# Kernel tuning notes

Measured on AMD Instinct MI355X. Metric: run time of the kernel, lower is better.

The kernel has to match this reference:

```python
import jax, jax.numpy as jnp
import numpy as np
from jax import lax

N = 100000   # n_nodes
E = 600000   # n_edges (no self loops by construction)
D = 128      # hidden_dim
L = 3        # n_hops
K = 5        # tail_k_threshold


def setup_inputs() -> dict:
    key = jax.random.key(0)
    ks = jax.random.split(key, 10)
    x = jax.random.normal(ks[0], (N, D), dtype=jnp.float32)
    src = jax.random.randint(ks[1], (E,), 0, N)
    off = jax.random.randint(ks[2], (E,), 1, N)
    dst = (src + off) % N  # guarantees dst != src (self loops removed in original)
    s = 1.0 / np.sqrt(D)
    def U(k, shape):
        return jax.random.uniform(k, shape, minval=-s, maxval=s, dtype=jnp.float32)
    return {
        "x": x,
        "G1": U(ks[3], (L, D, D)), "G2": U(ks[4], (L, D, D)),
        "B1": U(ks[5], (L, D, D)), "B2": U(ks[6], (L, D, D)),
        "R": U(ks[7], (L, D)),
        "edge_src": src, "edge_dst": dst,
    }


def _lrelu(v):
    return jax.nn.leaky_relu(v, 0.2)


def reference(x, G1, G2, B1, B2, R, edge_src, edge_dst):
    # row degrees of adj (A[src, dst] = 1)
    deg = jax.ops.segment_sum(jnp.ones(E, jnp.float32), edge_src, num_segments=N)
    inv_d = jnp.where(deg > 0, 1.0 / jnp.maximum(deg, 1.0), 0.0)   # left norm D^-1 A
    inv_d1 = 1.0 / (deg + 1.0)                                      # (A+I) left norm
    inv_d2 = 1.0 / (deg + 2.0)                                      # +1 virtual node
    w0, w1, w2 = inv_d[edge_src], inv_d1[edge_src], inv_d2[edge_src]
    head_mask = deg > K

    def spmm(w_edge, h):  # (D^-1 A) @ h via gather-scale-scatter
        return jax.ops.segment_sum(w_edge[:, None] * h[edge_dst], edge_src, num_segments=N)

    def propagate(head):
        h = x
        embs = [h]
        sups = []
        for l in range(L):
            nb = spmm(w0, h)
            ft = lax.stop_gradient(h)
            nbd = lax.stop_gradient(nb)
            gamma = _lrelu(ft @ G1[l].T + nbd @ G2[l].T) + 1.0
            beta = _lrelu(ft @ B1[l].T + nbd @ B2[l].T)
            m = ft + gamma * R[l] + beta - nbd   # missing_info (Relation, ablation=0)
            sups.append(m)
            if head:
                h = spmm(w1, h) + inv_d1[:, None] * h
            else:
                h = spmm(w2, h) + inv_d2[:, None] * h + m * inv_d2[:, None]
            embs.append(h)
        emb = jnp.mean(jnp.stack(embs, 0), 0)
        sup = jnp.mean(jnp.stack(sups, 0), 0)
        return emb, sup

    emb_h, _ = propagate(True)
    emb_t, _ = propagate(False)
    node_emb = jnp.where(head_mask[:, None], emb_h, emb_t)
    return node_emb
```

## Files before the change

### kernel.cpp

```cpp
#include <hip/hip_runtime.h>

#define N_NODES 100000
#define N_EDGES 600000
#define DIM 128
#define SCAN_B 1024
#define NCHUNK 98

typedef __attribute__((ext_vector_type(4))) float f32x4;
typedef __attribute__((ext_vector_type(8))) short bf16x8;
typedef __attribute__((ext_vector_type(4))) unsigned short u16x4;
typedef __attribute__((ext_vector_type(8))) unsigned short u16x8;

__device__ __forceinline__ unsigned short f2bf(float f) {
    union { float f; unsigned u; } cv; cv.f = f;
    unsigned r = (cv.u + 0x7FFFu + ((cv.u >> 16) & 1u)) >> 16;
    return (unsigned short)r;
}
__device__ __forceinline__ float bf2f(unsigned short v) {
    union { unsigned u; float f; } c; c.u = ((unsigned)v) << 16; return c.f;
}


__global__ void k_degree(const int* __restrict__ src, int* __restrict__ degi) {
    int e = blockIdx.x * 256 + threadIdx.x;
    if (e < N_EDGES) atomicAdd(&degi[src[e]], 1);
}

__global__ void k_chunksum(const int* __restrict__ degi, int* __restrict__ bsum) {
    __shared__ int sm[SCAN_B];
    int i = blockIdx.x * SCAN_B + threadIdx.x;
    sm[threadIdx.x] = (i < N_NODES) ? degi[i] : 0;
    __syncthreads();
    for (int s = SCAN_B / 2; s > 0; s >>= 1) {
        if (threadIdx.x < (unsigned)s) sm[threadIdx.x] += sm[threadIdx.x + s];
        __syncthreads();
    }
    if (threadIdx.x == 0) bsum[blockIdx.x] = sm[0];
}

__global__ void k_scanb(int* __restrict__ bsum, int nb) {
    __shared__ int sm[128];
    int t = threadIdx.x;
    int v = (t < nb) ? bsum[t] : 0;
    sm[t] = v; __syncthreads();
    for (int s = 1; s < 128; s <<= 1) {
        int a = (t >= s) ? sm[t - s] : 0;
        __syncthreads();
        sm[t] += a;
        __syncthreads();
    }
    if (t < nb) bsum[t] = sm[t] - v;
}

__global__ void k_rowptr(const int* __restrict__ degi, const int* __restrict__ bsum,
                         int* __restrict__ rowptr, int* __restrict__ cnt,
                         float* __restrict__ inv0, float* __restrict__ inv1,
                         float* __restrict__ inv2) {
    __shared__ int sm[SCAN_B];
    int i = blockIdx.x * SCAN_B + threadIdx.x;
    int v = (i < N_NODES) ? degi[i] : 0;
    sm[threadIdx.x] = v; __syncthreads();
    for (int s = 1; s < SCAN_B; s <<= 1) {
        int a = (threadIdx.x >= (unsigned)s) ? sm[threadIdx.x - s] : 0;
        __syncthreads();
        sm[threadIdx.x] += a;
        __syncthreads();
    }
    if (i < N_NODES) {
        int excl = bsum[blockIdx.x] + sm[threadIdx.x] - v;
        rowptr[i] = excl;
        cnt[i] = excl;
        float d = (float)v;
        inv0[i] = (v > 0) ? 1.0f / d : 0.0f;
        inv1[i] = 1.0f / (d + 1.0f);
        inv2[i] = 1.0f / (d + 2.0f);
    }
}

__global__ void k_fill(const int* __restrict__ src, const int* __restrict__ dst,
                       int* __restrict__ cnt, int* __restrict__ col) {
    int e = blockIdx.x * 256 + threadIdx.x;
    if (e < N_EDGES) {
        int pos = atomicAdd(&cnt[src[e]], 1);
        col[pos] = dst[e];
    }
}

__global__ void k_pack(const float* __restrict__ G1, const float* __restrict__ G2,
                       const float* __restrict__ B1, const float* __restrict__ B2,
                       short* __restrict__ Wp) {
    int idx = blockIdx.x * 256 + threadIdx.x;
    int j = idx & 7, lane = (idx >> 3) & 63, nt = (idx >> 9) & 15, kb = (idx >> 13) & 7, l = idx >> 16;
    int k = kb * 32 + (lane >> 4) * 8 + j;
    int n = nt * 16 + (lane & 15);
    float v;
    if (n < 128) {
        v = (k < 128) ? G1[(l * 128 + n) * 128 + k] : G2[(l * 128 + n) * 128 + (k - 128)];
    } else {
        int n2 = n - 128;
        v = (k < 128) ? B1[(l * 128 + n2) * 128 + k] : B2[(l * 128 + n2) * 128 + (k - 128)];
    }
    Wp[idx] = (short)f2bf(v);
}

__global__ void k_xcast(const float* __restrict__ x, unsigned short* __restrict__ xb) {
    int i = (blockIdx.x * 256 + threadIdx.x) * 4;
    f32x4 v = *(const f32x4*)(x + i);
    unsigned short o0 = f2bf(v[0]), o1 = f2bf(v[1]), o2 = f2bf(v[2]), o3 = f2bf(v[3]);
    unsigned long long pk = (unsigned long long)o0 | ((unsigned long long)o1 << 16)
                          | ((unsigned long long)o2 << 32) | ((unsigned long long)o3 << 48);
    *(unsigned long long*)(xb + i) = pk;
}


__device__ __forceinline__ void gather4(const u16x8* __restrict__ h8,
        const int* __restrict__ col, int start, int d, int lane, float* acc) {
    int c = lane & 15;
    int base = lane & 48;
    int dd = d < 16 ? d : 16;
    int idx = (c < dd) ? col[start + c] : 0;
    int dm = d;
    int tmx = __shfl_xor(dm, 16);
    dm = dm > tmx ? dm : tmx;
    tmx = __shfl_xor(dm, 32);
    dm = dm > tmx ? dm : tmx;
    int dmain = dm < 16 ? dm : 16;
    int e = 0;
    for (; e + 2 <= dmain; e += 2) {
        int c0 = __shfl(idx, base + e, 64);
        int c1 = __shfl(idx, base + e + 1, 64);
        if (e < d) {
            u16x8 v = h8[(size_t)c0 * 16 + c];
#pragma unroll
            for (int j = 0; j < 8; ++j) acc[j] += bf2f(v[j]);
        }
        if (e + 1 < d) {
            u16x8 v = h8[(size_t)c1 * 16 + c];
#pragma unroll
            for (int j = 0; j < 8; ++j) acc[j] += bf2f(v[j]);
        }
    }
    if (e < dmain) {
        int c0 = __shfl(idx, base + e, 64);
        if (e < d) {
            u16x8 v = h8[(size_t)c0 * 16 + c];
#pragma unroll
            for (int j = 0; j < 8; ++j) acc[j] += bf2f(v[j]);
        }
        ++e;
    }
    if (dm > 16) {
        for (; e < d; ++e) {
            int c0 = col[start + e];
            u16x8 v = h8[(size_t)c0 * 16 + c];
#pragma unroll
            for (int j = 0; j < 8; ++j) acc[j] += bf2f(v[j]);
        }
    }
}

__global__ __launch_bounds__(256) void k_agg0(
    const unsigned short* __restrict__ xb, unsigned short* __restrict__ Sb,
    unsigned short* __restrict__ hA, const float* __restrict__ inv1,
    const int* __restrict__ rowptr, const int* __restrict__ degi,
    const int* __restrict__ col)
{
    int lane = threadIdx.x & 63;
    int wid = (blockIdx.x * 256 + threadIdx.x) >> 6;
    int g = lane >> 4, c = lane & 15;
    int row = wid * 4 + g;
    int start = rowptr[row], d = degi[row];
    float acc[8] = {0,0,0,0,0,0,0,0};
    gather4((const u16x8*)xb, col, start, d, lane, acc);
    u16x8 hv = ((const u16x8*)xb)[(size_t)row * 16 + c];
    float w = inv1[row];
    u16x8 so, ho;
#pragma unroll
    for (int j = 0; j < 8; ++j) {
        so[j] = f2bf(acc[j]);
        ho[j] = f2bf(w * (acc[j] + bf2f(hv[j])));
    }
    ((u16x8*)Sb)[(size_t)row * 16 + c] = so;
    ((u16x8*)hA)[(size_t)row * 16 + c] = ho;
}

__global__ __launch_bounds__(256) void k_agg_head4(
    const unsigned short* __restrict__ hsrc, unsigned short* __restrict__ hnext,
    const unsigned short* __restrict__ xb, const unsigned short* __restrict__ h1b,
    float* __restrict__ outp, const float* __restrict__ inv1,
    const int* __restrict__ rowptr, const int* __restrict__ degi,
    const int* __restrict__ col, int final_hop)
{
    int lane = threadIdx.x & 63;
    int wid = (blockIdx.x * 256 + threadIdx.x) >> 6;
    int g = lane >> 4, c = lane & 15;
    int row = wid * 4 + g;
    int start = rowptr[row], d = degi[row];
    float acc[8] = {0,0,0,0,0,0,0,0};
    gather4((const u16x8*)hsrc, col, start, d, lane, acc);
    u16x8 hv = ((const u16x8*)hsrc)[(size_t)row * 16 + c];
    float w = inv1[row];
    float hn[8];
#pragma unroll
    for (int j = 0; j < 8; ++j) hn[j] = w * (acc[j] + bf2f(hv[j]));
    if (!final_hop) {
        u16x8 ho;
#pragma unroll
        for (int j = 0; j < 8; ++j) ho[j] = f2bf(hn[j]);
        ((u16x8*)hnext)[(size_t)row * 16 + c] = ho;
    } else {
        u16x8 xv = ((const u16x8*)xb)[(size_t)row * 16 + c];
        u16x8 h1 = ((const u16x8*)h1b)[(size_t)row * 16 + c];
        f32x4 e0, e1;
#pragma unroll
        for (int j = 0; j < 4; ++j)
            e0[j] = 0.25f * (bf2f(xv[j]) + bf2f(h1[j]) + bf2f(hv[j]) + hn[j]);
#pragma unroll
        for (int j = 0; j < 4; ++j)
            e1[j] = 0.25f * (bf2f(xv[4 + j]) + bf2f(h1[4 + j]) + bf2f(hv[4 + j]) + hn[4 + j]);
        float* op = outp + (size_t)row * DIM + c * 8;
        *(f32x4*)op = e0;
        *(f32x4*)(op + 4) = e1;
    }
}

__global__ __launch_bounds__(256) void k_agg_tail4(
    const unsigned short* __restrict__ hsrc, unsigned short* __restrict__ Sb,
    const int* __restrict__ rowptr, const int* __restrict__ degi,
    const int* __restrict__ col)
{
    int lane = threadIdx.x & 63;
    int wid = (blockIdx.x * 256 + threadIdx.x) >> 6;
    int g = lane >> 4, c = lane & 15;
    int row = wid * 4 + g;
    int start = rowptr[row], d = degi[row];
    float acc[8] = {0,0,0,0,0,0,0,0};
    gather4((const u16x8*)hsrc, col, start, d, lane, acc);
    u16x8 so;
#pragma unroll
    for (int j = 0; j < 8; ++j) so[j] = f2bf(acc[j]);
    ((u16x8*)Sb)[(size_t)row * 16 + c] = so;
}

__global__ __launch_bounds__(256) void k_gemm_tail(
    const unsigned short* __restrict__ hb, const unsigned short* __restrict__ Sb,
    unsigned short* __restrict__ hb_next,
    const unsigned short* __restrict__ xb, const unsigned short* __restrict__ h1b,
    float* __restrict__ outp,
    const float* __restrict__ Rl, const short* __restrict__ Wp,
    const float* __restrict__ inv0, const float* __restrict__ inv2,
    const int* __restrict__ degi, int last)
{
    __shared__ __align__(16) char smraw[33792];
    short* smW = (short*)smraw;
    float (*zb)[8][264] = (float(*)[8][264])smraw;

    int wave = threadIdx.x >> 6, lane = threadIdx.x & 63;
    int quad = lane >> 4, m16 = lane & 15;
    int r0 = blockIdx.x * 64 + wave * 16;
    int rowA = r0 + m16;
    int cA = rowA < N_NODES ? rowA : N_NODES - 1;
    float w0 = inv0[cA];
    const unsigned short* hrow = hb + (size_t)cA * DIM;
    const unsigned short* srow = Sb + (size_t)cA * DIM;

    f32x4 acc[16];
    const f32x4 vz = {0.f, 0.f, 0.f, 0.f};
#pragma unroll
    for (int t = 0; t < 16; ++t) acc[t] = vz;

    {
        const int4* g = (const int4*)Wp;
        int4* sd = (int4*)smW;
#pragma unroll
        for (int j = 0; j < 4; ++j) sd[j * 256 + threadIdx.x] = g[j * 256 + threadIdx.x];
    }

#pragma unroll
    for (int kb = 0; kb < 8; ++kb) {
        bf16x8 a;
        if (kb < 4) {
            a = *(const bf16x8*)(hrow + kb * 32 + quad * 8);
        } else {
            u16x8 sv = *(const u16x8*)(srow + (kb - 4) * 32 + quad * 8);
#pragma unroll
            for (int j = 0; j < 8; ++j) a[j] = (short)f2bf(w0 * bf2f(sv[j]));
        }
        __syncthreads();
        if (kb < 7) {
            const int4* g = (const int4*)(Wp + (kb + 1) * 8192);
            int4* sd = (int4*)(smW + ((kb + 1) & 1) * 8192);
#pragma unroll
            for (int j = 0; j < 4; ++j) sd[j * 256 + threadIdx.x] = g[j * 256 + threadIdx.x];
        }
        const short* wb = smW + (kb & 1) * 8192 + lane * 8;
#pragma unroll
        for (int nt = 0; nt < 16; ++nt) {
            bf16x8 b = *(const bf16x8*)(wb + nt * 512);
            acc[nt] = __builtin_amdgcn_mfma_f32_16x16x32_bf16(a, b, acc[nt], 0, 0, 0);
        }
    }
    __syncthreads();

    int c4 = (lane & 31) * 4;
    int halfsel = lane >> 5;
    f32x4 Rv = *(const f32x4*)(Rl + c4);

#pragma unroll
    for (int s = 0; s < 2; ++s) {
        if ((quad >> 1) == s) {
            int lr = (quad & 1) * 4;
#pragma unroll
            for (int nt = 0; nt < 16; ++nt)
#pragma unroll
                for (int r = 0; r < 4; ++r)
                    zb[wave][lr + r][nt * 16 + m16] = acc[nt][r];
        }
        __syncthreads();
#pragma unroll
        for (int it = 0; it < 4; ++it) {
            int lr = it * 2 + halfsel;
            int gi = r0 + s * 8 + lr;
            if (gi < N_NODES) {
                f32x4 z1 = *(const f32x4*)&zb[wave][lr][c4];
                f32x4 z2 = *(const f32x4*)&zb[wave][lr][128 + c4];
                u16x4 hu = *(const u16x4*)(hb + (size_t)gi * DIM + c4);
                u16x4 su = *(const u16x4*)(Sb + (size_t)gi * DIM + c4);
                float wi0 = inv0[gi], wi2 = inv2[gi];
                f32x4 hn, hvf;
#pragma unroll
                for (int j = 0; j < 4; ++j) {
                    float h = bf2f(hu[j]);
                    float sva = bf2f(su[j]);
                    float nb = wi0 * sva;
                    float g = (z1[j] > 0.f ? z1[j] : 0.2f * z1[j]) + 1.0f;
                    float be = (z2[j] > 0.f ? z2[j] : 0.2f * z2[j]);
                    float mm = h + g * Rv[j] + be - nb;
                    hn[j] = wi2 * (sva + h + mm);
                    hvf[j] = h;
                }
                if (!last) {
                    u16x4 o;
#pragma unroll
                    for (int j = 0; j < 4; ++j) o[j] = f2bf(hn[j]);
                    *(u16x4*)(hb_next + (size_t)gi * DIM + c4) = o;
                } else if (degi[gi] <= 5) {
                    u16x4 xu  = *(const u16x4*)(xb  + (size_t)gi * DIM + c4);
                    u16x4 h1u = *(const u16x4*)(h1b + (size_t)gi * DIM + c4);
                    f32x4 ev;
#pragma unroll
                    for (int j = 0; j < 4; ++j)
                        ev[j] = 0.25f * (bf2f(xu[j]) + bf2f(h1u[j]) + hvf[j] + hn[j]);
                    *(f32x4*)(outp + (size_t)gi * DIM + c4) = ev;
                }
            }
        }
        __syncthreads();
    }
}


extern "C" void kernel_launch(void* const* d_in, const int* in_sizes, int n_in,
                              void* d_out, int out_size, void* d_ws, size_t ws_size,
                              hipStream_t stream) {
    const float* x  = (const float*)d_in[0];
    const float* G1 = (const float*)d_in[1];
    const float* G2 = (const float*)d_in[2];
    const float* B1 = (const float*)d_in[3];
    const float* B2 = (const float*)d_in[4];
    const float* R  = (const float*)d_in[5];
    const int* esrc = (const int*)d_in[6];
    const int* edst = (const int*)d_in[7];
    float* out = (float*)d_out;

    char* base = (char*)d_ws;
    size_t off = 0;
    auto alloc = [&](size_t b) -> void* {
        void* p = base + off;
        off = (off + b + 255) & ~(size_t)255;
        return p;
    };
    int* degi   = (int*)alloc(4 * N_NODES);
    int* rowptr = (int*)alloc(4 * N_NODES);
    int* cnt    = (int*)alloc(4 * N_NODES);
    int* bsum   = (int*)alloc(4 * 256);
    int* col    = (int*)alloc(4 * N_EDGES);
    float* inv0 = (float*)alloc(4 * N_NODES);
    float* inv1 = (float*)alloc(4 * N_NODES);
    float* inv2 = (float*)alloc(4 * N_NODES);
    short* Wp   = (short*)alloc(2 * 3 * 65536);
    unsigned short* xb = (unsigned short*)alloc(2ull * N_NODES * DIM);
    unsigned short* hA = (unsigned short*)alloc(2ull * N_NODES * DIM);
    unsigned short* hB = (unsigned short*)alloc(2ull * N_NODES * DIM);
    unsigned short* tA = (unsigned short*)alloc(2ull * N_NODES * DIM);
    unsigned short* Sb = (unsigned short*)alloc(2ull * N_NODES * DIM);

    hipMemsetAsync(degi, 0, 4 * N_NODES, stream);
    k_degree<<<(N_EDGES + 255) / 256, 256, 0, stream>>>(esrc, degi);
    k_chunksum<<<NCHUNK, SCAN_B, 0, stream>>>(degi, bsum);
    k_scanb<<<1, 128, 0, stream>>>(bsum, NCHUNK);
    k_rowptr<<<NCHUNK, SCAN_B, 0, stream>>>(degi, bsum, rowptr, cnt, inv0, inv1, inv2);
    k_fill<<<(N_EDGES + 255) / 256, 256, 0, stream>>>(esrc, edst, cnt, col);
    k_pack<<<768, 256, 0, stream>>>(G1, G2, B1, B2, Wp);
    k_xcast<<<12500, 256, 0, stream>>>(x, xb);

    k_agg0<<<6250, 256, 0, stream>>>(xb, Sb, hA, inv1, rowptr, degi, col);
    k_gemm_tail<<<1563, 256, 0, stream>>>(xb, Sb, tA, xb, tA, out, R, Wp, inv0, inv2, degi, 0);

    k_agg_head4<<<6250, 256, 0, stream>>>(hA, hB, xb, hA, out, inv1, rowptr, degi, col, 0);
    k_agg_head4<<<6250, 256, 0, stream>>>(hB, hB, xb, hA, out, inv1, rowptr, degi, col, 1);

    k_agg_tail4<<<6250, 256, 0, stream>>>(tA, Sb, rowptr, degi, col);
    k_gemm_tail<<<1563, 256, 0, stream>>>(tA, Sb, hB, xb, tA, out, R + 128, Wp + 65536, inv0, inv2, degi, 0);
    k_agg_tail4<<<6250, 256, 0, stream>>>(hB, Sb, rowptr, degi, col);
    k_gemm_tail<<<1563, 256, 0, stream>>>(hB, Sb, hB, xb, tA, out, R + 256, Wp + 131072, inv0, inv2, degi, 1);
}
```

Before: 481.5 us.

## Drop LDS staging in tail GEMM; read weights from global, epilogue from registers

The tail GEMM kernel no longer stages weight tiles through shared memory with double buffering. Each lane now loads its B fragments directly from global memory (cached in L2), and s_barrier calls keep the waves roughly in step. The epilogue runs straight from the MFMA accumulator registers, so the shared-memory transpose and its syncthreads are gone, and launch_bounds(256,4) is added to raise occupancy. The cost is scattered 2-byte global loads and stores in the epilogue, which coalesce worse than the old vectorized 4-wide accesses, and per-lane global weight reads that may add latency.

```diff
diff --git a/kernel.cpp b/kernel.cpp
--- a/kernel.cpp
+++ b/kernel.cpp
@@ -242,7 +242,7 @@
     ((u16x8*)Sb)[(size_t)row * 16 + c] = so;
 }
 
-__global__ __launch_bounds__(256) void k_gemm_tail(
+__global__ __launch_bounds__(256, 4) void k_gemm_tail(
     const unsigned short* __restrict__ hb, const unsigned short* __restrict__ Sb,
     unsigned short* __restrict__ hb_next,
     const unsigned short* __restrict__ xb, const unsigned short* __restrict__ h1b,
@@ -251,18 +251,15 @@
     const float* __restrict__ inv0, const float* __restrict__ inv2,
     const int* __restrict__ degi, int last)
 {
-    __shared__ __align__(16) char smraw[33792];
-    short* smW = (short*)smraw;
-    float (*zb)[8][264] = (float(*)[8][264])smraw;
-
     int wave = threadIdx.x >> 6, lane = threadIdx.x & 63;
     int quad = lane >> 4, m16 = lane & 15;
     int r0 = blockIdx.x * 64 + wave * 16;
     int rowA = r0 + m16;
     int cA = rowA < N_NODES ? rowA : N_NODES - 1;
     float w0 = inv0[cA];
-    const unsigned short* hrow = hb + (size_t)cA * DIM;
-    const unsigned short* srow = Sb + (size_t)cA * DIM;
+    const unsigned short* hrow = hb + (size_t)cA * DIM + quad * 8;
+    const unsigned short* srow = Sb + (size_t)cA * DIM + quad * 8;
+    const short* wlane = Wp + lane * 8;
 
     f32x4 acc[16];
     const f32x4 vz = {0.f, 0.f, 0.f, 0.f};
@@ -270,92 +267,81 @@
     for (int t = 0; t < 16; ++t) acc[t] = vz;
 
     {
-        const int4* g = (const int4*)Wp;
-        int4* sd = (int4*)smW;
-#pragma unroll
-        for (int j = 0; j < 4; ++j) sd[j * 256 + threadIdx.x] = g[j * 256 + threadIdx.x];
-    }
-
-#pragma unroll
-    for (int kb = 0; kb < 8; ++kb) {
-        bf16x8 a;
-        if (kb < 4) {
-            a = *(const bf16x8*)(hrow + kb * 32 + quad * 8);
-        } else {
-            u16x8 sv = *(const u16x8*)(srow + (kb - 4) * 32 + quad * 8);
+        bf16x8 ah[4];
+#pragma unroll
+        for (int kb = 0; kb < 4; ++kb) ah[kb] = *(const bf16x8*)(hrow + kb * 32);
+#pragma unroll
+        for (int kb = 0; kb < 4; ++kb) {
+#pragma unroll
+            for (int nt = 0; nt < 16; ++nt) {
+                bf16x8 b = *(const bf16x8*)(wlane + (kb * 16 + nt) * 512);
+                acc[nt] = __builtin_amdgcn_mfma_f32_16x16x32_bf16(ah[kb], b, acc[nt], 0, 0, 0);
+            }
+            __builtin_amdgcn_s_barrier();
+        }
+    }
+    {
+        bf16x8 as[4];
+#pragma unroll
+        for (int kb = 0; kb < 4; ++kb) {
+            u16x8 sv = *(const u16x8*)(srow + kb * 32);
+            bf16x8 a;
 #pragma unroll
             for (int j = 0; j < 8; ++j) a[j] = (short)f2bf(w0 * bf2f(sv[j]));
-        }
-        __syncthreads();
-        if (kb < 7) {
-            const int4* g = (const int4*)(Wp + (kb + 1) * 8192);
-            int4* sd = (int4*)(smW + ((kb + 1) & 1) * 8192);
-#pragma unroll
-            for (int j = 0; j < 4; ++j) sd[j * 256 + threadIdx.x] = g[j * 256 + threadIdx.x];
-        }
-        const short* wb = smW + (kb & 1) * 8192 + lane * 8;
-#pragma unroll
-        for (int nt = 0; nt < 16; ++nt) {
-            bf16x8 b = *(const bf16x8*)(wb + nt * 512);
-            acc[nt] = __builtin_amdgcn_mfma_f32_16x16x32_bf16(a, b, acc[nt], 0, 0, 0);
-        }
-    }
-    __syncthreads();
-
-    int c4 = (lane & 31) * 4;
-    int halfsel = lane >> 5;
-    f32x4 Rv = *(const f32x4*)(Rl + c4);
-
-#pragma unroll
-    for (int s = 0; s < 2; ++s) {
-        if ((quad >> 1) == s) {
-            int lr = (quad & 1) * 4;
-#pragma unroll
-            for (int nt = 0; nt < 16; ++nt)
-#pragma unroll
-                for (int r = 0; r < 4; ++r)
-                    zb[wave][lr + r][nt * 16 + m16] = acc[nt][r];
-        }
-        __syncthreads();
-#pragma unroll
-        for (int it = 0; it < 4; ++it) {
-            int lr = it * 2 + halfsel;
-            int gi = r0 + s * 8 + lr;
-            if (gi < N_NODES) {
-                f32x4 z1 = *(const f32x4*)&zb[wave][lr][c4];
-                f32x4 z2 = *(const f32x4*)&zb[wave][lr][128 + c4];
-                u16x4 hu = *(const u16x4*)(hb + (size_t)gi * DIM + c4);
-                u16x4 su = *(const u16x4*)(Sb + (size_t)gi * DIM + c4);
-                float wi0 = inv0[gi], wi2 = inv2[gi];
-                f32x4 hn, hvf;
-#pragma unroll
-                for (int j = 0; j < 4; ++j) {
-                    float h = bf2f(hu[j]);
-                    float sva = bf2f(su[j]);
-                    float nb = wi0 * sva;
-                    float g = (z1[j] > 0.f ? z1[j] : 0.2f * z1[j]) + 1.0f;
-                    float be = (z2[j] > 0.f ? z2[j] : 0.2f * z2[j]);
-                    float mm = h + g * Rv[j] + be - nb;
-                    hn[j] = wi2 * (sva + h + mm);
-                    hvf[j] = h;
+            as[kb] = a;
+        }
+#pragma unroll
+        for (int kb = 0; kb < 4; ++kb) {
+#pragma unroll
+            for (int nt = 0; nt < 16; ++nt) {
+                bf16x8 b = *(const bf16x8*)(wlane + ((kb + 4) * 16 + nt) * 512);
+                acc[nt] = __builtin_amdgcn_mfma_f32_16x16x32_bf16(as[kb], b, acc[nt], 0, 0, 0);
+            }
+            if (kb < 3) __builtin_amdgcn_s_barrier();
+        }
+    }
+
+    float Rv[8];
+#pragma unroll
+    for (int nt = 0; nt < 8; ++nt) Rv[nt] = Rl[nt * 16 + m16];
+
+#pragma unroll
+    for (int r = 0; r < 4; ++r) {
+        int gi = r0 + quad * 4 + r;
+        if (gi < N_NODES) {
+            float wi0 = inv0[gi], wi2 = inv2[gi];
+            const unsigned short* hE = hb + (size_t)gi * DIM + m16;
+            const unsigned short* sE = Sb + (size_t)gi * DIM + m16;
+            if (!last) {
+                unsigned short* oE = hb_next + (size_t)gi * DIM + m16;
+#pragma unroll
+                for (int nt = 0; nt < 8; ++nt) {
+                    float z1 = acc[nt][r], z2 = acc[nt + 8][r];
+                    float h = bf2f(hE[nt * 16]);
+                    float sva = bf2f(sE[nt * 16]);
+                    float g = (z1 > 0.f ? z1 : 0.2f * z1) + 1.0f;
+                    float be = (z2 > 0.f ? z2 : 0.2f * z2);
+                    float mm = h + g * Rv[nt] + be - wi0 * sva;
+                    float hn = wi2 * (sva + h + mm);
+                    oE[nt * 16] = f2bf(hn);
                 }
-                if (!last) {
-                    u16x4 o;
-#pragma unroll
-                    for (int j = 0; j < 4; ++j) o[j] = f2bf(hn[j]);
-                    *(u16x4*)(hb_next + (size_t)gi * DIM + c4) = o;
-                } else if (degi[gi] <= 5) {
-                    u16x4 xu  = *(const u16x4*)(xb  + (size_t)gi * DIM + c4);
-                    u16x4 h1u = *(const u16x4*)(h1b + (size_t)gi * DIM + c4);
-                    f32x4 ev;
-#pragma unroll
-                    for (int j = 0; j < 4; ++j)
-                        ev[j] = 0.25f * (bf2f(xu[j]) + bf2f(h1u[j]) + hvf[j] + hn[j]);
-                    *(f32x4*)(outp + (size_t)gi * DIM + c4) = ev;
+            } else if (degi[gi] <= 5) {
+                const unsigned short* xE = xb + (size_t)gi * DIM + m16;
+                const unsigned short* h1E = h1b + (size_t)gi * DIM + m16;
+                float* oE = outp + (size_t)gi * DIM + m16;
+#pragma unroll
+                for (int nt = 0; nt < 8; ++nt) {
+                    float z1 = acc[nt][r], z2 = acc[nt + 8][r];
+                    float h = bf2f(hE[nt * 16]);
+                    float sva = bf2f(sE[nt * 16]);
+                    float g = (z1 > 0.f ? z1 : 0.2f * z1) + 1.0f;
+                    float be = (z2 > 0.f ? z2 : 0.2f * z2);
+                    float mm = h + g * Rv[nt] + be - wi0 * sva;
+                    float hn = wi2 * (sva + h + mm);
+                    oE[nt * 16] = 0.25f * (bf2f(xE[nt * 16]) + bf2f(h1E[nt * 16]) + h + hn);
                 }
             }
         }
-        __syncthreads();
     }
 }
 
```

Measured after the change: 483.7 us. No clear change (+0.4%).
